# Kernel tuning notes

Hardware: AMD Instinct MI355X
Metric: run time of the kernel (lower is better)

Reference implementation:

```python
import jax, jax.numpy as jnp
import numpy as np

MAX_LEN = 2048

def setup_inputs() -> dict:
    key = jax.random.key(0)
    k1, k2, k3 = jax.random.split(key, 3)
    B, S, E, V, C = 32, 2048, 512, 50257, 2
    x = jax.random.randint(k1, (B, S), 0, V, dtype=jnp.int64)
    emb_table = jax.random.normal(k2, (V, E), dtype=jnp.float32) * 0.02
    fc_w = jax.random.normal(k3, (C, E), dtype=jnp.float32) * 0.02
    fc_b = jnp.zeros((C,), dtype=jnp.float32)
    return {"x": x, "emb_table": emb_table, "fc_w": fc_w, "fc_b": fc_b}

def reference(x, emb_table, fc_w, fc_b):
    x = x[:, :MAX_LEN]                               # [B,S]
    x_emb = emb_table[x]                             # [B,S,E]
    scores = jnp.einsum('bse,bte->bst', x_emb, x_emb)  # [B,S,S] unscaled
    attn = jax.nn.softmax(scores, axis=-1)
    attended = jnp.einsum('bst,bte->bse', attn, x_emb)  # [B,S,E]
    pooled = attended.max(axis=1)                    # pool='max' -> [B,E]
    return pooled @ fc_w.T + fc_b                    # [B,C]
```

## Files before the change

### kernel.cpp

```cpp
#include <hip/hip_runtime.h>
#include <float.h>


typedef __attribute__((ext_vector_type(8))) short short8;
typedef __attribute__((ext_vector_type(4))) float f32x4;
typedef __attribute__((ext_vector_type(16))) float f32x16;
typedef __attribute__((ext_vector_type(4))) short s16x4;

__device__ __forceinline__ short f2bf(float f) {
  unsigned u = __float_as_uint(f);
  unsigned r = (u + 0x7fffu + ((u >> 16) & 1u)) >> 16;
  return (short)r;
}
__device__ __forceinline__ float bf2f(short s) {
  return __uint_as_float(((unsigned)(unsigned short)s) << 16);
}
__device__ __forceinline__ unsigned f2e4m3(float f) {
  unsigned u = __float_as_uint(f);
  unsigned s = (u >> 31) << 7;
  int exp = (int)((u >> 23) & 0xff) - 127;
  unsigned m = (u & 0x7fffff) | 0x800000;
  if (exp < -10) return s;
  int shift = 20, e4 = 0;
  if (exp >= -6) e4 = exp + 7;
  else shift += (-6 - exp);
  unsigned keep = m >> shift;
  unsigned rem = m & ((1u << shift) - 1u);
  unsigned half = 1u << (shift - 1);
  keep += (rem > half || (rem == half && (keep & 1)));
  unsigned out;
  if (e4 > 0) {
    if (keep >= 16) { keep >>= 1; e4++; }
    out = ((unsigned)e4 << 3) | (keep & 7);
  } else {
    out = (keep >= 8) ? ((1u << 3) | (keep & 7)) : keep;
  }
  return s | out;
}
__device__ __forceinline__ unsigned ordf(float f) {
  unsigned u = __float_as_uint(f);
  return (u & 0x80000000u) ? ~u : (u | 0x80000000u);
}
__device__ __forceinline__ float unordf(unsigned e) {
  unsigned u = (e & 0x80000000u) ? (e ^ 0x80000000u) : ~e;
  return __uint_as_float(u);
}
__device__ __forceinline__ void gload16(const void* g, void* s) {
  __builtin_amdgcn_global_load_lds((const __attribute__((address_space(1))) void*)g,
                                   (__attribute__((address_space(3))) void*)s,
                                   16, 0, 0);
}
__device__ __forceinline__ unsigned pkbf(float lo, float hi) {
  unsigned r;
  asm("v_cvt_pk_bf16_f32 %0, %1, %2" : "=v"(r) : "v"(lo), "v"(hi));
  return r;
}
#define PLSWAP(a, b) asm volatile("v_permlane32_swap_b32 %0, %1" : "+v"(a), "+v"(b))
__device__ __forceinline__ long long mklong(unsigned lo, unsigned hi) {
  return (long long)((((unsigned long long)hi) << 32) | lo);
}

extern "C" __global__ __launch_bounds__(256)
void prep4(const int* __restrict__ xp, const float* __restrict__ emb,
           unsigned char* __restrict__ Kf8, short* __restrict__ Vf) {
  __shared__ __align__(16) short ls[32 * 520];
  const int t = threadIdx.x, kt = blockIdx.x, b = blockIdx.y;
  {
    const int r = t >> 3, seg = t & 7;
    const float* src = emb + (long)xp[b * 2048 + kt * 32 + r] * 512 + seg * 64;
    short* ldst = ls + r * 520 + seg * 64;
#pragma unroll
    for (int i = 0; i < 8; ++i) {
      float4 fa = *(const float4*)(src + i * 8);
      float4 fb = *(const float4*)(src + i * 8 + 4);
      short8 v = { f2bf(fa.x), f2bf(fa.y), f2bf(fa.z), f2bf(fa.w),
                   f2bf(fb.x), f2bf(fb.y), f2bf(fb.z), f2bf(fb.w) };
      *(short8*)(ldst + i * 8) = v;
    }
  }
  __syncthreads();
  {
    const long chunkK = ((long)b * 64 + kt) * 16384;
#pragma unroll
    for (int i = 0; i < 4; ++i) {
      int j = t * 4 + i;
      int sp = j >> 6, lj = j & 63;
      int keyl = lj & 31, hi2 = lj >> 5;
      const short* row = ls + keyl * 520 + 8 * hi2;
      unsigned dw[4];
#pragma unroll
      for (int c2 = 0; c2 < 4; ++c2) {
        unsigned d = 0;
#pragma unroll
        for (int bb2 = 0; bb2 < 4; ++bb2) {
          int c = c2 * 4 + bb2;
          int e = 16 * (2 * sp + (c >> 3)) + (c & 7);
          d |= f2e4m3(bf2f(row[e])) << (8 * bb2);
        }
        dw[c2] = d;
      }
      *(uint4*)(Kf8 + chunkK + (long)j * 16) = (uint4){dw[0], dw[1], dw[2], dw[3]};
    }
  }
#pragma unroll
  for (int rr = 0; rr < 8; ++rr) {
    int j = rr * 256 + t;
    int eb = j >> 7, ks2 = (j >> 6) & 1, l = j & 63;
    int e32 = l & 31, hi = l >> 5;
    const short* colp = ls + (ks2 * 16 + hi * 8) * 520 + eb * 32 + e32;
    short8 v = { colp[0], colp[520], colp[1040], colp[1560],
                 colp[2080], colp[2600], colp[3120], colp[3640] };
    *(short8*)(Vf + ((long)(b * 2048 + eb * 128 + kt * 2 + ks2) * 64 + l) * 8) = v;
  }
}

extern "C" __global__ __launch_bounds__(512, 2)
void attn7(const unsigned char* __restrict__ Kf8, const short* __restrict__ Vf,
           unsigned* __restrict__ pooled) {
  __shared__ __align__(16) uint4 lq8[32 * 64];
  __shared__ __align__(16) uint4 lp4[2][32 * 64];
  __shared__ float lsm[512];

  const int t = threadIdx.x, l = t & 63, w = t >> 6;
  const int n = blockIdx.x;
  const int b = (n & 7) + ((n >> 8) << 3);
  const int qt = (n >> 3) & 31;
  const int q32 = l & 31, hi = l >> 5;

  {
    const unsigned char* src = Kf8 + ((long)b * 64 + 2 * qt) * 16384;
#pragma unroll
    for (int i = 0; i < 4; ++i) {
      int sw = i * 512 + w * 64;
      gload16(src + (long)(sw + l) * 16, lq8 + sw);
    }
  }

  const unsigned char* kc0 = Kf8 + ((long)b * 64 + w) * 16384 + (long)l * 16;
  const short* vp0 = Vf + ((long)(b * 2048 + (2 * w) * 128) * 64 + l) * 8;

#define LOADK8(dst, base, half)                                               \
  {                                                                           \
    _Pragma("unroll") for (int i = 0; i < 8; ++i)                             \
        dst[i] = *(const uint4*)((base) + ((half) * 8 + i) * 1024);           \
  }
#define QK8(kv, sp)                                                           \
  {                                                                           \
    long long ak0 = mklong(kv.x, kv.y);                                       \
    long long ak1 = mklong(kv.z, kv.w);                                       \
    uint4 qa = lq8[(sp) * 64 + l];                                            \
    uint4 qb = lq8[(16 + (sp)) * 64 + l];                                     \
    S0 = __builtin_amdgcn_mfma_f32_32x32x16_fp8_fp8(ak0, mklong(qa.x, qa.y), S0, 0, 0, 0); \
    S1 = __builtin_amdgcn_mfma_f32_32x32x16_fp8_fp8(ak0, mklong(qb.x, qb.y), S1, 0, 0, 0); \
    S0 = __builtin_amdgcn_mfma_f32_32x32x16_fp8_fp8(ak1, mklong(qa.z, qa.w), S0, 0, 0, 0); \
    S1 = __builtin_amdgcn_mfma_f32_32x32x16_fp8_fp8(ak1, mklong(qb.z, qb.w), S1, 0, 0, 0); \
  }

  uint4 kA[8], kB[8];
  LOADK8(kA, kc0, 0)
  LOADK8(kB, kc0, 1)
  __syncthreads();

  f32x16 acc[2][2];
#pragma unroll
  for (int eg = 0; eg < 2; ++eg)
#pragma unroll
    for (int qg = 0; qg < 2; ++qg)
#pragma unroll
      for (int r = 0; r < 16; ++r) acc[eg][qg][r] = 0.f;
  float lr0 = 0.f, lr1 = 0.f;
  int buf = 0;

  for (int kt = 0; kt < 8; ++kt) {
    f32x16 S0, S1;
#pragma unroll
    for (int r = 0; r < 16; ++r) { S0[r] = 0.f; S1[r] = 0.f; }
    __builtin_amdgcn_s_setprio(1);
#pragma unroll
    for (int sp = 0; sp < 8; ++sp) QK8(kA[sp], sp)
#pragma unroll
    for (int sp = 0; sp < 8; ++sp) QK8(kB[sp], 8 + sp)
    __builtin_amdgcn_s_setprio(0);

    float ps0 = 0.f, ps1 = 0.f;
#pragma unroll
    for (int r = 0; r < 16; ++r) {
      S0[r] = __expf(S0[r]); ps0 += S0[r];
      S1[r] = __expf(S1[r]); ps1 += S1[r];
    }
    lr0 += ps0; lr1 += ps1;

    const short* vp = vp0 + (long)(kt * 16) * 512;
    short8 vb[8];
#pragma unroll
    for (int ks = 0; ks < 4; ++ks) {
      vb[2 * ks]     = *(const short8*)(vp + ks * 512);
      vb[2 * ks + 1] = *(const short8*)(vp + 128 * 512 + ks * 512);
    }
    {
      const int nkt = (kt < 7) ? kt + 1 : 7;
      const unsigned char* kcn = kc0 + (long)nkt * 131072;
      LOADK8(kA, kcn, 0)
      LOADK8(kB, kcn, 1)
    }

    {
      unsigned a0 = pkbf(S0[0], S0[1]),   c0 = pkbf(S0[4], S0[5]);   PLSWAP(a0, c0);
      unsigned a1 = pkbf(S0[2], S0[3]),   c1 = pkbf(S0[6], S0[7]);   PLSWAP(a1, c1);
      unsigned a2 = pkbf(S0[8], S0[9]),   c2 = pkbf(S0[12], S0[13]); PLSWAP(a2, c2);
      unsigned a3 = pkbf(S0[10], S0[11]), c3 = pkbf(S0[14], S0[15]); PLSWAP(a3, c3);
      lp4[buf][(4 * w + 0) * 64 + l] = (uint4){a0, a1, c0, c1};
      lp4[buf][(4 * w + 2) * 64 + l] = (uint4){a2, a3, c2, c3};
      unsigned d0 = pkbf(S1[0], S1[1]),   e0 = pkbf(S1[4], S1[5]);   PLSWAP(d0, e0);
      unsigned d1 = pkbf(S1[2], S1[3]),   e1 = pkbf(S1[6], S1[7]);   PLSWAP(d1, e1);
      unsigned d2 = pkbf(S1[8], S1[9]),   e2 = pkbf(S1[12], S1[13]); PLSWAP(d2, e2);
      unsigned d3 = pkbf(S1[10], S1[11]), e3 = pkbf(S1[14], S1[15]); PLSWAP(d3, e3);
      lp4[buf][(4 * w + 1) * 64 + l] = (uint4){d0, d1, e0, e1};
      lp4[buf][(4 * w + 3) * 64 + l] = (uint4){d2, d3, e2, e3};
    }
    asm volatile("s_waitcnt lgkmcnt(0)" ::: "memory");
    __builtin_amdgcn_s_barrier();

    const short* lps = (const short*)lp4[buf];
#pragma unroll
    for (int ks = 0; ks < 16; ++ks) {
      short8 v0 = vb[(ks & 3) * 2];
      short8 v1 = vb[(ks & 3) * 2 + 1];
      short8 pf0 = *(const short8*)(lps + ((ks * 2 + 0) * 64 + l) * 8);
      short8 pf1 = *(const short8*)(lps + ((ks * 2 + 1) * 64 + l) * 8);
      __builtin_amdgcn_s_setprio(1);
      acc[0][0] = __builtin_amdgcn_mfma_f32_32x32x16_bf16(v0, pf0, acc[0][0], 0, 0, 0);
      acc[0][1] = __builtin_amdgcn_mfma_f32_32x32x16_bf16(v0, pf1, acc[0][1], 0, 0, 0);
      acc[1][0] = __builtin_amdgcn_mfma_f32_32x32x16_bf16(v1, pf0, acc[1][0], 0, 0, 0);
      acc[1][1] = __builtin_amdgcn_mfma_f32_32x32x16_bf16(v1, pf1, acc[1][1], 0, 0, 0);
      __builtin_amdgcn_s_setprio(0);
      if (ks < 12) {
        vb[(ks & 3) * 2]     = *(const short8*)(vp + (ks + 4) * 512);
        vb[(ks & 3) * 2 + 1] = *(const short8*)(vp + 128 * 512 + (ks + 4) * 512);
      }
    }
    buf ^= 1;
  }

  lr0 += __shfl_xor(lr0, 32, 64);
  lr1 += __shfl_xor(lr1, 32, 64);
  __syncthreads();
  if (l < 32) {
    lsm[w * 32 + l] = lr0;
    lsm[256 + w * 32 + l] = lr1;
  }
  __syncthreads();
  float lt0 = lsm[q32], lt1 = lsm[256 + q32];
#pragma unroll
  for (int kg = 1; kg < 8; ++kg) {
    lt0 += lsm[kg * 32 + q32];
    lt1 += lsm[256 + kg * 32 + q32];
  }
  float ri0 = 1.0f / lt0, ri1 = 1.0f / lt1;
#pragma unroll
  for (int eg = 0; eg < 2; ++eg)
#pragma unroll
    for (int r = 0; r < 16; ++r) {
      float v = fmaxf(acc[eg][0][r] * ri0, acc[eg][1][r] * ri1);
      v = fmaxf(v, __shfl_xor(v, 1, 64));
      v = fmaxf(v, __shfl_xor(v, 2, 64));
      v = fmaxf(v, __shfl_xor(v, 4, 64));
      v = fmaxf(v, __shfl_xor(v, 8, 64));
      v = fmaxf(v, __shfl_xor(v, 16, 64));
      if (q32 == 0) {
        int e = (2 * w + eg) * 32 + (r & 3) + 8 * (r >> 2) + 4 * hi;
        atomicMax(&pooled[b * 512 + e], ordf(v));
      }
    }
}

#define LDKp 520
#define LDVp 40
#define LDPp 40
extern "C" __global__ __launch_bounds__(256, 2)
void attn_fb(const int* __restrict__ xp, const float* __restrict__ emb,
             unsigned* __restrict__ pooled) {
  __shared__ __align__(16) short lds_k[32 * LDKp];
  __shared__ __align__(16) short lds_vt[512 * LDVp];
  __shared__ __align__(16) short lds_p[64 * LDPp];
  const int t = threadIdx.x, l = t & 63, w = t >> 6;
  const int b = blockIdx.y;
  const int q0 = blockIdx.x * 64;
  const int L = l & 15, g = l >> 4;
  short8 qf[16];
  {
    int qq = q0 + w * 16 + L;
    const float* qrow = emb + (long)xp[b * 2048 + qq] * 512;
#pragma unroll
    for (int ec = 0; ec < 16; ++ec) {
      int e0 = ec * 32 + 8 * g;
      float4 fa = *(const float4*)(qrow + e0);
      float4 fb = *(const float4*)(qrow + e0 + 4);
      short8 v = { f2bf(fa.x), f2bf(fa.y), f2bf(fa.z), f2bf(fa.w),
                   f2bf(fb.x), f2bf(fb.y), f2bf(fb.z), f2bf(fb.w) };
      qf[ec] = v;
    }
  }
  f32x4 acc[32];
#pragma unroll
  for (int nt = 0; nt < 32; ++nt) acc[nt] = (f32x4){0.f, 0.f, 0.f, 0.f};
  float mrun[4] = {-FLT_MAX, -FLT_MAX, -FLT_MAX, -FLT_MAX};
  float lrun[4] = {0.f, 0.f, 0.f, 0.f};
  for (int kt = 0; kt < 64; ++kt) {
    __syncthreads();
    if (t < 128) {
#pragma unroll 4
      for (int i = 0; i < 32; ++i) {
        const float* krow = emb + (long)xp[b * 2048 + kt * 32 + i] * 512;
        float4 f = *(const float4*)(krow + 4 * t);
        s16x4 v = { f2bf(f.x), f2bf(f.y), f2bf(f.z), f2bf(f.w) };
        *(s16x4*)&lds_k[i * LDKp + 4 * t] = v;
      }
    } else {
      const int u = t - 128, lane_ = u & 63, half = u >> 6;
#pragma unroll 2
      for (int kq = 0; kq < 8; ++kq) {
        const int kbase = b * 2048 + kt * 32 + kq * 4;
        const float* r0 = emb + (long)xp[kbase + 0] * 512;
        const float* r1 = emb + (long)xp[kbase + 1] * 512;
        const float* r2 = emb + (long)xp[kbase + 2] * 512;
        const float* r3 = emb + (long)xp[kbase + 3] * 512;
#pragma unroll
        for (int seg = 0; seg < 4; ++seg) {
          int e = lane_ + 64 * (seg + 4 * half);
          s16x4 v = { f2bf(r0[e]), f2bf(r1[e]), f2bf(r2[e]), f2bf(r3[e]) };
          *(s16x4*)&lds_vt[e * LDVp + 4 * kq] = v;
        }
      }
    }
    __syncthreads();
    f32x4 s0 = {0.f, 0.f, 0.f, 0.f}, s1 = {0.f, 0.f, 0.f, 0.f};
#pragma unroll
    for (int ec = 0; ec < 16; ++ec) {
      short8 k0 = *(const short8*)&lds_k[L * LDKp + ec * 32 + 8 * g];
      short8 k1 = *(const short8*)&lds_k[(L + 16) * LDKp + ec * 32 + 8 * g];
      s0 = __builtin_amdgcn_mfma_f32_16x16x32_bf16(qf[ec], k0, s0, 0, 0, 0);
      s1 = __builtin_amdgcn_mfma_f32_16x16x32_bf16(qf[ec], k1, s1, 0, 0, 0);
    }
    float p0[4], p1[4], sc[4];
#pragma unroll
    for (int r = 0; r < 4; ++r) {
      float v = fmaxf(s0[r], s1[r]);
      v = fmaxf(v, __shfl_xor(v, 1, 64));
      v = fmaxf(v, __shfl_xor(v, 2, 64));
      v = fmaxf(v, __shfl_xor(v, 4, 64));
      v = fmaxf(v, __shfl_xor(v, 8, 64));
      float nm = fmaxf(mrun[r], v);
      sc[r] = expf(mrun[r] - nm);
      p0[r] = expf(s0[r] - nm);
      p1[r] = expf(s1[r] - nm);
      float rs = p0[r] + p1[r];
      rs += __shfl_xor(rs, 1, 64);
      rs += __shfl_xor(rs, 2, 64);
      rs += __shfl_xor(rs, 4, 64);
      rs += __shfl_xor(rs, 8, 64);
      lrun[r] = lrun[r] * sc[r] + rs;
      mrun[r] = nm;
    }
    if (__any(sc[0] < 1.f || sc[1] < 1.f || sc[2] < 1.f || sc[3] < 1.f)) {
      f32x4 sv = { sc[0], sc[1], sc[2], sc[3] };
#pragma unroll
      for (int nt = 0; nt < 32; ++nt) acc[nt] *= sv;
    }
#pragma unroll
    for (int r = 0; r < 4; ++r) {
      int row = w * 16 + g * 4 + r;
      lds_p[row * LDPp + L]      = f2bf(p0[r]);
      lds_p[row * LDPp + 16 + L] = f2bf(p1[r]);
    }
    asm volatile("s_waitcnt lgkmcnt(0)" ::: "memory");
    short8 pf = *(const short8*)&lds_p[(w * 16 + L) * LDPp + 8 * g];
#pragma unroll
    for (int nt = 0; nt < 32; ++nt) {
      short8 vf = *(const short8*)&lds_vt[(nt * 16 + L) * LDVp + 8 * g];
      acc[nt] = __builtin_amdgcn_mfma_f32_16x16x32_bf16(pf, vf, acc[nt], 0, 0, 0);
    }
  }
  __syncthreads();
  float inv[4];
#pragma unroll
  for (int r = 0; r < 4; ++r) inv[r] = 1.f / lrun[r];
  float* rbuf = (float*)lds_k;
#pragma unroll
  for (int nt = 0; nt < 32; ++nt) {
    f32x4 a = acc[nt];
    float c = fmaxf(fmaxf(a[0] * inv[0], a[1] * inv[1]),
                    fmaxf(a[2] * inv[2], a[3] * inv[3]));
    c = fmaxf(c, __shfl_xor(c, 16, 64));
    c = fmaxf(c, __shfl_xor(c, 32, 64));
    if (g == 0) rbuf[w * 512 + nt * 16 + L] = c;
  }
  __syncthreads();
  for (int j = t; j < 512; j += 256) {
    float v = fmaxf(fmaxf(rbuf[j], rbuf[512 + j]),
                    fmaxf(rbuf[1024 + j], rbuf[1536 + j]));
    atomicMax(&pooled[b * 512 + j], ordf(v));
  }
}

extern "C" __global__ void fc_small(const unsigned* __restrict__ pooled,
                                    const float* __restrict__ fw,
                                    const float* __restrict__ fb,
                                    float* __restrict__ out) {
  int t = threadIdx.x;
  if (t >= 64) return;
  int bb = t >> 1, c = t & 1;
  float s = fb[c];
  for (int e = 0; e < 512; ++e)
    s += unordf(pooled[bb * 512 + e]) * fw[c * 512 + e];
  out[t] = s;
}

extern "C" void kernel_launch(void* const* d_in, const int* in_sizes, int n_in,
                              void* d_out, int out_size, void* d_ws, size_t ws_size,
                              hipStream_t stream) {
  const int* xp    = (const int*)d_in[0];
  const float* emb = (const float*)d_in[1];
  const float* fw  = (const float*)d_in[2];
  const float* fb  = (const float*)d_in[3];
  unsigned* pooled = (unsigned*)d_ws;

  hipMemsetAsync(pooled, 0, 32 * 512 * sizeof(unsigned), stream);

  const size_t need = 65536ull + 33554432ull + 2ull * 33554432ull * sizeof(short);
  if (ws_size >= need) {
    unsigned char* Kf8 = (unsigned char*)d_ws + 65536;
    short* Vff = (short*)(Kf8 + 33554432);
    prep4<<<dim3(64, 32), 256, 0, stream>>>(xp, emb, Kf8, Vff);
    attn7<<<dim3(1024), 512, 0, stream>>>(Kf8, Vff, pooled);
  } else {
    attn_fb<<<dim3(32, 32), 256, 0, stream>>>(xp, emb, pooled);
  }
  fc_small<<<1, 64, 0, stream>>>(pooled, fw, fb, (float*)d_out);
}
```

Before: 310.7 us.

## Software-pipeline QK and PV MFMAs across key tiles in attention loop

Restructures the attention main loop so the PV matmul for tile kt-1 is interleaved with the QK matmul for tile kt, with a prologue and epilogue for the first and last tiles. K and V register loads are issued per step inside the interleaved loop rather than in bulk, and V prefetch now streams continuously across tiles. The aim is to keep the matrix units busy while exp/pack and barrier work would otherwise stall them. The cost is higher register pressure from live S, acc, kA/kB and vb together, which may cause spills under the 2-blocks-per-CU launch bound.

```diff
diff --git a/kernel.cpp b/kernel.cpp
--- a/kernel.cpp
+++ b/kernel.cpp
@@ -115,7 +115,7 @@
 }
 
 extern "C" __global__ __launch_bounds__(512, 2)
-void attn7(const unsigned char* __restrict__ Kf8, const short* __restrict__ Vf,
+void attn9(const unsigned char* __restrict__ Kf8, const short* __restrict__ Vf,
            unsigned* __restrict__ pooled) {
   __shared__ __align__(16) uint4 lq8[32 * 64];
   __shared__ __align__(16) uint4 lp4[2][32 * 64];
@@ -137,13 +137,9 @@
   }
 
   const unsigned char* kc0 = Kf8 + ((long)b * 64 + w) * 16384 + (long)l * 16;
-  const short* vp0 = Vf + ((long)(b * 2048 + (2 * w) * 128) * 64 + l) * 8;
-
-#define LOADK8(dst, base, half)                                               \
-  {                                                                           \
-    _Pragma("unroll") for (int i = 0; i < 8; ++i)                             \
-        dst[i] = *(const uint4*)((base) + ((half) * 8 + i) * 1024);           \
-  }
+  const short* vpA = Vf + ((long)(b * 2048 + (2 * w) * 128) * 64 + l) * 8;
+  const short* vpB = vpA + 128 * 512;
+
 #define QK8(kv, sp)                                                           \
   {                                                                           \
     long long ak0 = mklong(kv.x, kv.y);                                       \
@@ -155,10 +151,35 @@
     S0 = __builtin_amdgcn_mfma_f32_32x32x16_fp8_fp8(ak1, mklong(qa.z, qa.w), S0, 0, 0, 0); \
     S1 = __builtin_amdgcn_mfma_f32_32x32x16_fp8_fp8(ak1, mklong(qb.z, qb.w), S1, 0, 0, 0); \
   }
+#define PACK2(pb)                                                             \
+  {                                                                           \
+    unsigned a0 = pkbf(S0[0], S0[1]),   c0 = pkbf(S0[4], S0[5]);   PLSWAP(a0, c0); \
+    unsigned a1 = pkbf(S0[2], S0[3]),   c1 = pkbf(S0[6], S0[7]);   PLSWAP(a1, c1); \
+    unsigned a2 = pkbf(S0[8], S0[9]),   c2 = pkbf(S0[12], S0[13]); PLSWAP(a2, c2); \
+    unsigned a3 = pkbf(S0[10], S0[11]), c3 = pkbf(S0[14], S0[15]); PLSWAP(a3, c3); \
+    lp4[pb][(4 * w + 0) * 64 + l] = (uint4){a0, a1, c0, c1};                  \
+    lp4[pb][(4 * w + 2) * 64 + l] = (uint4){a2, a3, c2, c3};                  \
+    unsigned d0 = pkbf(S1[0], S1[1]),   e0 = pkbf(S1[4], S1[5]);   PLSWAP(d0, e0); \
+    unsigned d1 = pkbf(S1[2], S1[3]),   e1 = pkbf(S1[6], S1[7]);   PLSWAP(d1, e1); \
+    unsigned d2 = pkbf(S1[8], S1[9]),   e2 = pkbf(S1[12], S1[13]); PLSWAP(d2, e2); \
+    unsigned d3 = pkbf(S1[10], S1[11]), e3 = pkbf(S1[14], S1[15]); PLSWAP(d3, e3); \
+    lp4[pb][(4 * w + 1) * 64 + l] = (uint4){d0, d1, e0, e1};                  \
+    lp4[pb][(4 * w + 3) * 64 + l] = (uint4){d2, d3, e2, e3};                  \
+  }
 
   uint4 kA[8], kB[8];
-  LOADK8(kA, kc0, 0)
-  LOADK8(kB, kc0, 1)
+#pragma unroll
+  for (int i = 0; i < 8; ++i) kA[i] = *(const uint4*)(kc0 + i * 1024);
+#pragma unroll
+  for (int i = 0; i < 8; ++i) kB[i] = *(const uint4*)(kc0 + (8 + i) * 1024);
+
+  short8 vb[8];
+#pragma unroll
+  for (int ks = 0; ks < 4; ++ks) {
+    vb[2 * ks]     = *(const short8*)(vpA + (long)ks * 512);
+    vb[2 * ks + 1] = *(const short8*)(vpB + (long)ks * 512);
+  }
+
   __syncthreads();
 
   f32x16 acc[2][2];
@@ -169,19 +190,26 @@
 #pragma unroll
       for (int r = 0; r < 16; ++r) acc[eg][qg][r] = 0.f;
   float lr0 = 0.f, lr1 = 0.f;
-  int buf = 0;
-
-  for (int kt = 0; kt < 8; ++kt) {
-    f32x16 S0, S1;
-#pragma unroll
-    for (int r = 0; r < 16; ++r) { S0[r] = 0.f; S1[r] = 0.f; }
+  f32x16 S0, S1;
+
+#pragma unroll
+  for (int r = 0; r < 16; ++r) { S0[r] = 0.f; S1[r] = 0.f; }
+  {
+    const unsigned char* kcn = kc0 + 131072;
     __builtin_amdgcn_s_setprio(1);
 #pragma unroll
-    for (int sp = 0; sp < 8; ++sp) QK8(kA[sp], sp)
-#pragma unroll
-    for (int sp = 0; sp < 8; ++sp) QK8(kB[sp], 8 + sp)
+    for (int sp = 0; sp < 8; ++sp) {
+      QK8(kA[sp], sp)
+      kA[sp] = *(const uint4*)(kcn + sp * 1024);
+    }
+#pragma unroll
+    for (int sp = 0; sp < 8; ++sp) {
+      QK8(kB[sp], 8 + sp)
+      kB[sp] = *(const uint4*)(kcn + (8 + sp) * 1024);
+    }
     __builtin_amdgcn_s_setprio(0);
-
+  }
+  {
     float ps0 = 0.f, ps1 = 0.f;
 #pragma unroll
     for (int r = 0; r < 16; ++r) {
@@ -189,45 +217,64 @@
       S1[r] = __expf(S1[r]); ps1 += S1[r];
     }
     lr0 += ps0; lr1 += ps1;
-
-    const short* vp = vp0 + (long)(kt * 16) * 512;
-    short8 vb[8];
-#pragma unroll
-    for (int ks = 0; ks < 4; ++ks) {
-      vb[2 * ks]     = *(const short8*)(vp + ks * 512);
-      vb[2 * ks + 1] = *(const short8*)(vp + 128 * 512 + ks * 512);
+  }
+  PACK2(0)
+  asm volatile("s_waitcnt lgkmcnt(0)" ::: "memory");
+  __builtin_amdgcn_s_barrier();
+
+  for (int kt = 1; kt < 8; ++kt) {
+    const short* lps = (const short*)lp4[(kt - 1) & 1];
+    const unsigned char* kcn = kc0 + (long)((kt < 7) ? kt + 1 : 7) * 131072;
+    const int base = (kt - 1) * 16;
+#pragma unroll
+    for (int r = 0; r < 16; ++r) { S0[r] = 0.f; S1[r] = 0.f; }
+#pragma unroll
+    for (int ks = 0; ks < 16; ++ks) {
+      short8 pf0 = *(const short8*)(lps + ((ks * 2 + 0) * 64 + l) * 8);
+      short8 pf1 = *(const short8*)(lps + ((ks * 2 + 1) * 64 + l) * 8);
+      short8 v0 = vb[(ks & 3) * 2];
+      short8 v1 = vb[(ks & 3) * 2 + 1];
+      __builtin_amdgcn_s_setprio(1);
+      acc[0][0] = __builtin_amdgcn_mfma_f32_32x32x16_bf16(v0, pf0, acc[0][0], 0, 0, 0);
+      acc[0][1] = __builtin_amdgcn_mfma_f32_32x32x16_bf16(v0, pf1, acc[0][1], 0, 0, 0);
+      acc[1][0] = __builtin_amdgcn_mfma_f32_32x32x16_bf16(v1, pf0, acc[1][0], 0, 0, 0);
+      acc[1][1] = __builtin_amdgcn_mfma_f32_32x32x16_bf16(v1, pf1, acc[1][1], 0, 0, 0);
+      if (ks < 8) {
+        QK8(kA[ks], ks)
+      } else {
+        QK8(kB[ks - 8], ks)
+      }
+      __builtin_amdgcn_s_setprio(0);
+      {
+        int nk = base + ks + 4; if (nk > 127) nk = 127;
+        vb[(ks & 3) * 2]     = *(const short8*)(vpA + (long)nk * 512);
+        vb[(ks & 3) * 2 + 1] = *(const short8*)(vpB + (long)nk * 512);
+      }
+      if (ks < 8) kA[ks] = *(const uint4*)(kcn + ks * 1024);
+      else        kB[ks - 8] = *(const uint4*)(kcn + ks * 1024);
     }
     {
-      const int nkt = (kt < 7) ? kt + 1 : 7;
-      const unsigned char* kcn = kc0 + (long)nkt * 131072;
-      LOADK8(kA, kcn, 0)
-      LOADK8(kB, kcn, 1)
-    }
-
-    {
-      unsigned a0 = pkbf(S0[0], S0[1]),   c0 = pkbf(S0[4], S0[5]);   PLSWAP(a0, c0);
-      unsigned a1 = pkbf(S0[2], S0[3]),   c1 = pkbf(S0[6], S0[7]);   PLSWAP(a1, c1);
-      unsigned a2 = pkbf(S0[8], S0[9]),   c2 = pkbf(S0[12], S0[13]); PLSWAP(a2, c2);
-      unsigned a3 = pkbf(S0[10], S0[11]), c3 = pkbf(S0[14], S0[15]); PLSWAP(a3, c3);
-      lp4[buf][(4 * w + 0) * 64 + l] = (uint4){a0, a1, c0, c1};
-      lp4[buf][(4 * w + 2) * 64 + l] = (uint4){a2, a3, c2, c3};
-      unsigned d0 = pkbf(S1[0], S1[1]),   e0 = pkbf(S1[4], S1[5]);   PLSWAP(d0, e0);
-      unsigned d1 = pkbf(S1[2], S1[3]),   e1 = pkbf(S1[6], S1[7]);   PLSWAP(d1, e1);
-      unsigned d2 = pkbf(S1[8], S1[9]),   e2 = pkbf(S1[12], S1[13]); PLSWAP(d2, e2);
-      unsigned d3 = pkbf(S1[10], S1[11]), e3 = pkbf(S1[14], S1[15]); PLSWAP(d3, e3);
-      lp4[buf][(4 * w + 1) * 64 + l] = (uint4){d0, d1, e0, e1};
-      lp4[buf][(4 * w + 3) * 64 + l] = (uint4){d2, d3, e2, e3};
-    }
+      float ps0 = 0.f, ps1 = 0.f;
+#pragma unroll
+      for (int r = 0; r < 16; ++r) {
+        S0[r] = __expf(S0[r]); ps0 += S0[r];
+        S1[r] = __expf(S1[r]); ps1 += S1[r];
+      }
+      lr0 += ps0; lr1 += ps1;
+    }
+    PACK2(kt & 1)
     asm volatile("s_waitcnt lgkmcnt(0)" ::: "memory");
     __builtin_amdgcn_s_barrier();
-
-    const short* lps = (const short*)lp4[buf];
+  }
+
+  {
+    const short* lps = (const short*)lp4[1];
 #pragma unroll
     for (int ks = 0; ks < 16; ++ks) {
+      short8 pf0 = *(const short8*)(lps + ((ks * 2 + 0) * 64 + l) * 8);
+      short8 pf1 = *(const short8*)(lps + ((ks * 2 + 1) * 64 + l) * 8);
       short8 v0 = vb[(ks & 3) * 2];
       short8 v1 = vb[(ks & 3) * 2 + 1];
-      short8 pf0 = *(const short8*)(lps + ((ks * 2 + 0) * 64 + l) * 8);
-      short8 pf1 = *(const short8*)(lps + ((ks * 2 + 1) * 64 + l) * 8);
       __builtin_amdgcn_s_setprio(1);
       acc[0][0] = __builtin_amdgcn_mfma_f32_32x32x16_bf16(v0, pf0, acc[0][0], 0, 0, 0);
       acc[0][1] = __builtin_amdgcn_mfma_f32_32x32x16_bf16(v0, pf1, acc[0][1], 0, 0, 0);
@@ -235,11 +282,11 @@
       acc[1][1] = __builtin_amdgcn_mfma_f32_32x32x16_bf16(v1, pf1, acc[1][1], 0, 0, 0);
       __builtin_amdgcn_s_setprio(0);
       if (ks < 12) {
-        vb[(ks & 3) * 2]     = *(const short8*)(vp + (ks + 4) * 512);
-        vb[(ks & 3) * 2 + 1] = *(const short8*)(vp + 128 * 512 + (ks + 4) * 512);
-      }
-    }
-    buf ^= 1;
+        int nk = 112 + ks + 4;
+        vb[(ks & 3) * 2]     = *(const short8*)(vpA + (long)nk * 512);
+        vb[(ks & 3) * 2 + 1] = *(const short8*)(vpB + (long)nk * 512);
+      }
+    }
   }
 
   lr0 += __shfl_xor(lr0, 32, 64);
@@ -432,7 +479,7 @@
     unsigned char* Kf8 = (unsigned char*)d_ws + 65536;
     short* Vff = (short*)(Kf8 + 33554432);
     prep4<<<dim3(64, 32), 256, 0, stream>>>(xp, emb, Kf8, Vff);
-    attn7<<<dim3(1024), 512, 0, stream>>>(Kf8, Vff, pooled);
+    attn9<<<dim3(1024), 512, 0, stream>>>(Kf8, Vff, pooled);
   } else {
     attn_fb<<<dim3(32, 32), 256, 0, stream>>>(xp, emb, pooled);
   }
```

New measurement: 312.1 us. No clear change (+0.5%).
